# Optimization experiments

Hardware: AMD Instinct MI355X
Metric: run time of the kernel (lower is better)

The kernel has to match this reference:

```python
import jax, jax.numpy as jnp
import numpy as np

B, H, W, C = 4, 64, 64, 64
DK = C // 8  # key/query channels from Conv2D(filters=channels//8)


def setup_inputs() -> dict:
    key = jax.random.key(0)
    ks = jax.random.split(key, 4)
    x = jax.random.normal(ks[0], (B, H, W, C), dtype=jnp.float32)
    # he_normal-ish scale for 1x1 conv kernels (fan_in = C)
    s = np.sqrt(2.0 / C).astype(np.float32)
    Wf = jax.random.normal(ks[1], (C, DK), dtype=jnp.float32) * s
    Wg = jax.random.normal(ks[2], (C, DK), dtype=jnp.float32) * s
    Wh = jax.random.normal(ks[3], (C, C), dtype=jnp.float32) * s
    bf = jnp.zeros((DK,), dtype=jnp.float32)
    bg = jnp.zeros((DK,), dtype=jnp.float32)
    bh = jnp.zeros((C,), dtype=jnp.float32)
    return {"x": x, "Wf": Wf, "bf": bf, "Wg": Wg, "bg": bg, "Wh": Wh, "bh": bh}


def reference(x, Wf, bf, Wg, bg, Wh, bh):
    b, h, w, c = x.shape
    n = h * w
    xf = x.reshape(b, n, c)  # 1x1 conv == per-position linear over flattened spatial dims
    f = xf @ Wf + bf         # [B, N, DK]
    g = xf @ Wg + bg         # [B, N, DK]
    v = xf @ Wh + bh         # [B, N, C]
    # attention = softmax(g @ f^T) over keys (tf.nn.softmax default: last axis)
    scores = jnp.einsum('bnd,bmd->bnm', g, f)   # [B, N, N]
    attn = jax.nn.softmax(scores, axis=-1)
    out = jnp.einsum('bnm,bmc->bnc', attn, v)   # [B, N, C]
    return out
```

## Files before the change

kernel.cpp:

```cpp
#include <hip/hip_runtime.h>
#include <hip/hip_bf16.h>
#include <hip/hip_fp16.h>

typedef _Float16 half8_t  __attribute__((ext_vector_type(8)));
typedef short    short8_t __attribute__((ext_vector_type(8)));
typedef short    short4_t __attribute__((ext_vector_type(4)));
typedef float    f32x4    __attribute__((ext_vector_type(4)));

#define LOG2E 1.44269504088896f

__device__ __forceinline__ unsigned pack_bf16_2(float lo, float hi) {
  float2 f2; f2.x = lo; f2.y = hi;
  __hip_bfloat162 h2 = __float22bfloat162_rn(f2);
  return *reinterpret_cast<unsigned*>(&h2);
}

__global__ __launch_bounds__(256) void prep_kernel(
    const float* __restrict__ x,
    const float* __restrict__ Wf, const float* __restrict__ bf,
    const float* __restrict__ Wg, const float* __restrict__ bg,
    const float* __restrict__ Wh, const float* __restrict__ bh,
    _Float16* __restrict__ fh, _Float16* __restrict__ gh,
    unsigned short* __restrict__ vT)
{
  __shared__ _Float16 WtT[80 * 72];
  __shared__ float ball[80];
  const int t = threadIdx.x;

  for (int i = t; i < 512; i += 256) {
    int c = i >> 3, d = i & 7;
    WtT[d * 72 + c]       = (_Float16)Wf[i];
    WtT[(8 + d) * 72 + c] = (_Float16)(Wg[i] * LOG2E);
  }
  for (int i = t; i < 4096; i += 256) {
    int c = i >> 6, ch = i & 63;
    WtT[(16 + ch) * 72 + c] = (_Float16)Wh[i];
  }
  if (t < 80) ball[t] = (t < 8) ? bf[t] : (t < 16) ? bg[t - 8] * LOG2E : bh[t - 16];
  __syncthreads();

  const int lane = t & 63, w = t >> 6;
  const int quad = lane >> 4, l15 = lane & 15;
  const int p0 = blockIdx.x * 64;
  const int row = p0 + w * 16 + l15;

  const float* xr = x + (size_t)row * 64 + quad * 8;
  float4 xa = *(const float4*)(xr);
  float4 xb = *(const float4*)(xr + 4);
  float4 xc = *(const float4*)(xr + 32);
  float4 xd = *(const float4*)(xr + 36);
  half8_t a0, a1;
  a0[0]=(_Float16)xa.x; a0[1]=(_Float16)xa.y; a0[2]=(_Float16)xa.z; a0[3]=(_Float16)xa.w;
  a0[4]=(_Float16)xb.x; a0[5]=(_Float16)xb.y; a0[6]=(_Float16)xb.z; a0[7]=(_Float16)xb.w;
  a1[0]=(_Float16)xc.x; a1[1]=(_Float16)xc.y; a1[2]=(_Float16)xc.z; a1[3]=(_Float16)xc.w;
  a1[4]=(_Float16)xd.x; a1[5]=(_Float16)xd.y; a1[6]=(_Float16)xd.z; a1[7]=(_Float16)xd.w;

  const f32x4 zc = {0.f, 0.f, 0.f, 0.f};
  const int b     = p0 >> 12;
  const int nbase = (p0 & 4095) + w * 16 + quad * 4;
  const int kblock = nbase >> 5;
  const int r0     = nbase & 31;
  const int q8 = r0 >> 3, j8 = r0 & 7;
  const int slot0 = (j8 < 4) ? (q8 * 4 + j8) : (16 + q8 * 4 + (j8 - 4));
  const size_t fbase_out = ((size_t)b * 4096 + (kblock << 5) + slot0) * 8;
  const size_t gbase_out = ((size_t)p0 + w * 16 + quad * 4) * 8;
  const size_t vbase_out = (((size_t)b * 128 + kblock) << 11) + r0;

#pragma unroll
  for (int nt = 0; nt < 5; nt++) {
    const int ch0 = nt * 16 + l15;
    const _Float16* wt = &WtT[ch0 * 72 + quad * 8];
    half8_t b0 = *(const half8_t*)(wt);
    half8_t b1 = *(const half8_t*)(wt + 32);
    f32x4 d = __builtin_amdgcn_mfma_f32_16x16x32_f16(a0, b0, zc, 0, 0, 0);
    d = __builtin_amdgcn_mfma_f32_16x16x32_f16(a1, b1, d, 0, 0, 0);
    const float bias = ball[ch0];
    if (nt == 0) {
      if (l15 < 8) {
#pragma unroll
        for (int reg = 0; reg < 4; reg++)
          fh[fbase_out + (size_t)reg * 8 + l15] = (_Float16)(d[reg] + bias);
      } else {
#pragma unroll
        for (int reg = 0; reg < 4; reg++)
          gh[gbase_out + (size_t)reg * 8 + (l15 - 8)] = (_Float16)(d[reg] + bias);
      }
    } else {
      const int vch = ch0 - 16;
      union { unsigned u[2]; short4_t s; } pk;
      pk.u[0] = pack_bf16_2(d[0] + bias, d[1] + bias);
      pk.u[1] = pack_bf16_2(d[2] + bias, d[3] + bias);
      *(short4_t*)(vT + vbase_out + (size_t)vch * 32) = pk.s;
    }
  }
}

__device__ __forceinline__ void compute_chunk(
    const half8_t& f0, const half8_t& f1,
    const short8_t& v0, const short8_t& v1,
    const short8_t& v2, const short8_t& v3,
    const half8_t (&gfrag)[4], const short8_t& ones8,
    f32x4 (&acc)[4][4], f32x4 (&acc4)[4])
{
  const f32x4 zc = {0.f, 0.f, 0.f, 0.f};
#pragma unroll
  for (int tt = 0; tt < 4; tt++) {
    f32x4 s0 = __builtin_amdgcn_mfma_f32_16x16x32_f16(f0, gfrag[tt], zc, 0, 0, 0);
    f32x4 s1 = __builtin_amdgcn_mfma_f32_16x16x32_f16(f1, gfrag[tt], zc, 0, 0, 0);
    float p00 = __builtin_amdgcn_exp2f(s0[0]), p01 = __builtin_amdgcn_exp2f(s0[1]);
    float p02 = __builtin_amdgcn_exp2f(s0[2]), p03 = __builtin_amdgcn_exp2f(s0[3]);
    float p10 = __builtin_amdgcn_exp2f(s1[0]), p11 = __builtin_amdgcn_exp2f(s1[1]);
    float p12 = __builtin_amdgcn_exp2f(s1[2]), p13 = __builtin_amdgcn_exp2f(s1[3]);
    union { unsigned u[4]; short8_t v; } pu;
    pu.u[0] = pack_bf16_2(p00, p01);
    pu.u[1] = pack_bf16_2(p02, p03);
    pu.u[2] = pack_bf16_2(p10, p11);
    pu.u[3] = pack_bf16_2(p12, p13);
    short8_t pfrag = pu.v;
    acc[tt][0] = __builtin_amdgcn_mfma_f32_16x16x32_bf16(v0, pfrag, acc[tt][0], 0, 0, 0);
    acc[tt][1] = __builtin_amdgcn_mfma_f32_16x16x32_bf16(v1, pfrag, acc[tt][1], 0, 0, 0);
    acc[tt][2] = __builtin_amdgcn_mfma_f32_16x16x32_bf16(v2, pfrag, acc[tt][2], 0, 0, 0);
    acc[tt][3] = __builtin_amdgcn_mfma_f32_16x16x32_bf16(v3, pfrag, acc[tt][3], 0, 0, 0);
    acc4[tt]   = __builtin_amdgcn_mfma_f32_16x16x32_bf16(ones8, pfrag, acc4[tt], 0, 0, 0);
  }
}

__global__ __launch_bounds__(512, 2) void attn_kernel(
    const _Float16* __restrict__ fh,
    const _Float16* __restrict__ gh,
    const unsigned short* __restrict__ vT,
    float* __restrict__ out)
{
  const int N    = 4096;
  const int lane = threadIdx.x & 63;
  const int w    = threadIdx.x >> 6;
  const int quad = lane >> 4;
  const int l15  = lane & 15;

  __shared__ float red[7][64][17];

  const int xcd = blockIdx.x & 7;
  const int b   = xcd >> 1;
  const int qg  = ((blockIdx.x >> 3) << 1) + (xcd & 1);
  const int q0  = qg * 64;
  const int kbase = w * 512;
  const int phase = (qg >> 1) & 15;

  const _Float16* fbase = fh + (size_t)b * N * 8;
  const _Float16* gbase = gh + (size_t)b * N * 8;
  const short*    vbat  = (const short*)vT + (size_t)b * 262144 + (l15 << 5) + (quad << 3);

  half8_t gfrag[4] = {{}, {}, {}, {}};
  if (quad == 0) {
#pragma unroll
    for (int tt = 0; tt < 4; tt++)
      gfrag[tt] = *(const half8_t*)(gbase + (size_t)(q0 + tt * 16 + l15) * 8);
  }

  const f32x4 zc = {0.f, 0.f, 0.f, 0.f};
  f32x4 acc[4][4];
  f32x4 acc4[4];
#pragma unroll
  for (int tt = 0; tt < 4; tt++) {
    acc4[tt] = zc;
#pragma unroll
    for (int ct = 0; ct < 4; ct++) acc[tt][ct] = zc;
  }

  short8_t ones8;
#pragma unroll
  for (int i = 0; i < 8; i++) ones8[i] = (short)0x3F80;

  half8_t  fa0 = {}, fa1 = {}, fb0 = {}, fb1 = {};
  short8_t va0, va1, va2, va3, vb0, vb1, vb2, vb3;

  {
    const int k0 = kbase + (((0 + phase) & 15) << 5);
    if (quad == 0) {
      fa0 = *(const half8_t*)(fbase + (size_t)(k0 + l15) * 8);
      fa1 = *(const half8_t*)(fbase + (size_t)(k0 + 16 + l15) * 8);
    }
    const short* vk = vbat + ((size_t)(k0 >> 5) << 11);
    va0 = *(const short8_t*)(vk);
    va1 = *(const short8_t*)(vk + 512);
    va2 = *(const short8_t*)(vk + 1024);
    va3 = *(const short8_t*)(vk + 1536);
  }

#pragma unroll 1
  for (int cc = 0; cc < 16; cc += 2) {
    {
      const int k1 = kbase + (((cc + 1 + phase) & 15) << 5);
      if (quad == 0) {
        fb0 = *(const half8_t*)(fbase + (size_t)(k1 + l15) * 8);
        fb1 = *(const half8_t*)(fbase + (size_t)(k1 + 16 + l15) * 8);
      }
      const short* vk = vbat + ((size_t)(k1 >> 5) << 11);
      vb0 = *(const short8_t*)(vk);
      vb1 = *(const short8_t*)(vk + 512);
      vb2 = *(const short8_t*)(vk + 1024);
      vb3 = *(const short8_t*)(vk + 1536);
    }
    compute_chunk(fa0, fa1, va0, va1, va2, va3, gfrag, ones8, acc, acc4);
    if (cc + 2 < 16) {
      const int k2 = kbase + (((cc + 2 + phase) & 15) << 5);
      if (quad == 0) {
        fa0 = *(const half8_t*)(fbase + (size_t)(k2 + l15) * 8);
        fa1 = *(const half8_t*)(fbase + (size_t)(k2 + 16 + l15) * 8);
      }
      const short* vk = vbat + ((size_t)(k2 >> 5) << 11);
      va0 = *(const short8_t*)(vk);
      va1 = *(const short8_t*)(vk + 512);
      va2 = *(const short8_t*)(vk + 1024);
      va3 = *(const short8_t*)(vk + 1536);
    }
    compute_chunk(fb0, fb1, vb0, vb1, vb2, vb3, gfrag, ones8, acc, acc4);
  }

#pragma unroll 1
  for (int tt = 0; tt < 4; tt++) {
    if (w > 0) {
      float* p = &red[w - 1][lane][0];
#pragma unroll
      for (int ct = 0; ct < 4; ct++)
#pragma unroll
        for (int reg = 0; reg < 4; reg++) p[ct * 4 + reg] = acc[tt][ct][reg];
      p[16] = acc4[tt][0];
    }
    __syncthreads();
    if (w == 0) {
      f32x4 a0 = acc[tt][0], a1 = acc[tt][1], a2 = acc[tt][2], a3 = acc[tt][3];
      float lv = acc4[tt][0];
#pragma unroll
      for (int ww = 0; ww < 7; ww++) {
        const float* p = &red[ww][lane][0];
#pragma unroll
        for (int reg = 0; reg < 4; reg++) {
          a0[reg] += p[0 + reg];
          a1[reg] += p[4 + reg];
          a2[reg] += p[8 + reg];
          a3[reg] += p[12 + reg];
        }
        lv += p[16];
      }
      const float inv = 1.0f / lv;
      float* ob = out + ((size_t)b * N + q0 + tt * 16 + l15) * 64 + (quad << 2);
      *(f32x4*)(ob)      = a0 * inv;
      *(f32x4*)(ob + 16) = a1 * inv;
      *(f32x4*)(ob + 32) = a2 * inv;
      *(f32x4*)(ob + 48) = a3 * inv;
    }
    __syncthreads();
  }
}

extern "C" void kernel_launch(void* const* d_in, const int* in_sizes, int n_in,
                              void* d_out, int out_size, void* d_ws, size_t ws_size,
                              hipStream_t stream) {
  const float* x  = (const float*)d_in[0];
  const float* Wf = (const float*)d_in[1];
  const float* bf = (const float*)d_in[2];
  const float* Wg = (const float*)d_in[3];
  const float* bg = (const float*)d_in[4];
  const float* Wh = (const float*)d_in[5];
  const float* bh = (const float*)d_in[6];
  float* out = (float*)d_out;

  char* ws = (char*)d_ws;
  _Float16* fh = (_Float16*)ws;
  _Float16* gh = (_Float16*)(ws + 262144);
  unsigned short* vT = (unsigned short*)(ws + 524288);

  prep_kernel<<<256, 256, 0, stream>>>(x, Wf, bf, Wg, bg, Wh, bh, fh, gh, vT);
  attn_kernel<<<256, 512, 0, stream>>>(fh, gh, vT, out);
}
```

Before: 100.4 us.

## Fuse projection and attention kernels via cooperative launch with grid sync

Merges the 1x1-conv projection prep kernel into the attention kernel and launches a single cooperative kernel, with a grid-wide barrier between the projection phase and the attention phase. The projection work per block is split across 8 waves instead of 4, and the shared memory for the weight staging is reused as the reduction buffer. The aim is to remove the second launch and the gap between kernels. In exchange it adds a grid sync, and it requires all 256 blocks of 512 threads to be co-resident, which could fail or serialize if occupancy is lower.

```diff
diff --git a/kernel.cpp b/kernel.cpp
--- a/kernel.cpp
+++ b/kernel.cpp
@@ -1,4 +1,5 @@
 #include <hip/hip_runtime.h>
+#include <hip/hip_cooperative_groups.h>
 #include <hip/hip_bf16.h>
 #include <hip/hip_fp16.h>
 
@@ -13,86 +14,6 @@
   float2 f2; f2.x = lo; f2.y = hi;
   __hip_bfloat162 h2 = __float22bfloat162_rn(f2);
   return *reinterpret_cast<unsigned*>(&h2);
-}
-
-__global__ __launch_bounds__(256) void prep_kernel(
-    const float* __restrict__ x,
-    const float* __restrict__ Wf, const float* __restrict__ bf,
-    const float* __restrict__ Wg, const float* __restrict__ bg,
-    const float* __restrict__ Wh, const float* __restrict__ bh,
-    _Float16* __restrict__ fh, _Float16* __restrict__ gh,
-    unsigned short* __restrict__ vT)
-{
-  __shared__ _Float16 WtT[80 * 72];
-  __shared__ float ball[80];
-  const int t = threadIdx.x;
-
-  for (int i = t; i < 512; i += 256) {
-    int c = i >> 3, d = i & 7;
-    WtT[d * 72 + c]       = (_Float16)Wf[i];
-    WtT[(8 + d) * 72 + c] = (_Float16)(Wg[i] * LOG2E);
-  }
-  for (int i = t; i < 4096; i += 256) {
-    int c = i >> 6, ch = i & 63;
-    WtT[(16 + ch) * 72 + c] = (_Float16)Wh[i];
-  }
-  if (t < 80) ball[t] = (t < 8) ? bf[t] : (t < 16) ? bg[t - 8] * LOG2E : bh[t - 16];
-  __syncthreads();
-
-  const int lane = t & 63, w = t >> 6;
-  const int quad = lane >> 4, l15 = lane & 15;
-  const int p0 = blockIdx.x * 64;
-  const int row = p0 + w * 16 + l15;
-
-  const float* xr = x + (size_t)row * 64 + quad * 8;
-  float4 xa = *(const float4*)(xr);
-  float4 xb = *(const float4*)(xr + 4);
-  float4 xc = *(const float4*)(xr + 32);
-  float4 xd = *(const float4*)(xr + 36);
-  half8_t a0, a1;
-  a0[0]=(_Float16)xa.x; a0[1]=(_Float16)xa.y; a0[2]=(_Float16)xa.z; a0[3]=(_Float16)xa.w;
-  a0[4]=(_Float16)xb.x; a0[5]=(_Float16)xb.y; a0[6]=(_Float16)xb.z; a0[7]=(_Float16)xb.w;
-  a1[0]=(_Float16)xc.x; a1[1]=(_Float16)xc.y; a1[2]=(_Float16)xc.z; a1[3]=(_Float16)xc.w;
-  a1[4]=(_Float16)xd.x; a1[5]=(_Float16)xd.y; a1[6]=(_Float16)xd.z; a1[7]=(_Float16)xd.w;
-
-  const f32x4 zc = {0.f, 0.f, 0.f, 0.f};
-  const int b     = p0 >> 12;
-  const int nbase = (p0 & 4095) + w * 16 + quad * 4;
-  const int kblock = nbase >> 5;
-  const int r0     = nbase & 31;
-  const int q8 = r0 >> 3, j8 = r0 & 7;
-  const int slot0 = (j8 < 4) ? (q8 * 4 + j8) : (16 + q8 * 4 + (j8 - 4));
-  const size_t fbase_out = ((size_t)b * 4096 + (kblock << 5) + slot0) * 8;
-  const size_t gbase_out = ((size_t)p0 + w * 16 + quad * 4) * 8;
-  const size_t vbase_out = (((size_t)b * 128 + kblock) << 11) + r0;
-
-#pragma unroll
-  for (int nt = 0; nt < 5; nt++) {
-    const int ch0 = nt * 16 + l15;
-    const _Float16* wt = &WtT[ch0 * 72 + quad * 8];
-    half8_t b0 = *(const half8_t*)(wt);
-    half8_t b1 = *(const half8_t*)(wt + 32);
-    f32x4 d = __builtin_amdgcn_mfma_f32_16x16x32_f16(a0, b0, zc, 0, 0, 0);
-    d = __builtin_amdgcn_mfma_f32_16x16x32_f16(a1, b1, d, 0, 0, 0);
-    const float bias = ball[ch0];
-    if (nt == 0) {
-      if (l15 < 8) {
-#pragma unroll
-        for (int reg = 0; reg < 4; reg++)
-          fh[fbase_out + (size_t)reg * 8 + l15] = (_Float16)(d[reg] + bias);
-      } else {
-#pragma unroll
-        for (int reg = 0; reg < 4; reg++)
-          gh[gbase_out + (size_t)reg * 8 + (l15 - 8)] = (_Float16)(d[reg] + bias);
-      }
-    } else {
-      const int vch = ch0 - 16;
-      union { unsigned u[2]; short4_t s; } pk;
-      pk.u[0] = pack_bf16_2(d[0] + bias, d[1] + bias);
-      pk.u[1] = pack_bf16_2(d[2] + bias, d[3] + bias);
-      *(short4_t*)(vT + vbase_out + (size_t)vch * 32) = pk.s;
-    }
-  }
 }
 
 __device__ __forceinline__ void compute_chunk(
@@ -125,19 +46,126 @@
   }
 }
 
-__global__ __launch_bounds__(512, 2) void attn_kernel(
-    const _Float16* __restrict__ fh,
-    const _Float16* __restrict__ gh,
-    const unsigned short* __restrict__ vT,
+__global__ __launch_bounds__(512, 2) void fused_kernel(
+    const float* __restrict__ x,
+    const float* __restrict__ Wf, const float* __restrict__ bf,
+    const float* __restrict__ Wg, const float* __restrict__ bg,
+    const float* __restrict__ Wh, const float* __restrict__ bh,
+    _Float16* __restrict__ fh, _Float16* __restrict__ gh,
+    unsigned short* __restrict__ vT,
     float* __restrict__ out)
 {
-  const int N    = 4096;
-  const int lane = threadIdx.x & 63;
-  const int w    = threadIdx.x >> 6;
+  namespace cg = cooperative_groups;
+  __shared__ __align__(16) char smraw[7 * 64 * 17 * 4];
+
+  const int t    = threadIdx.x;
+  const int lane = t & 63;
+  const int wv   = t >> 6;
   const int quad = lane >> 4;
   const int l15  = lane & 15;
 
-  __shared__ float red[7][64][17];
+  {
+    _Float16* WtT = (_Float16*)smraw;
+    float*    ball = (float*)(smraw + 80 * 72 * 2);
+
+    {
+      int i = t;
+      int c = i >> 3, d = i & 7;
+      WtT[d * 72 + c]       = (_Float16)Wf[i];
+      WtT[(8 + d) * 72 + c] = (_Float16)(Wg[i] * LOG2E);
+    }
+    for (int i = t; i < 4096; i += 512) {
+      int c = i >> 6, ch = i & 63;
+      WtT[(16 + ch) * 72 + c] = (_Float16)Wh[i];
+    }
+    if (t < 80) ball[t] = (t < 8) ? bf[t] : (t < 16) ? bg[t - 8] * LOG2E : bh[t - 16];
+    __syncthreads();
+
+    const int wr   = wv & 3;
+    const int half = wv >> 2;
+    const int p0  = blockIdx.x * 64;
+    const int row = p0 + wr * 16 + l15;
+
+    const float* xr = x + (size_t)row * 64 + quad * 8;
+    float4 xa = *(const float4*)(xr);
+    float4 xb = *(const float4*)(xr + 4);
+    float4 xc = *(const float4*)(xr + 32);
+    float4 xd = *(const float4*)(xr + 36);
+    half8_t a0, a1;
+    a0[0]=(_Float16)xa.x; a0[1]=(_Float16)xa.y; a0[2]=(_Float16)xa.z; a0[3]=(_Float16)xa.w;
+    a0[4]=(_Float16)xb.x; a0[5]=(_Float16)xb.y; a0[6]=(_Float16)xb.z; a0[7]=(_Float16)xb.w;
+    a1[0]=(_Float16)xc.x; a1[1]=(_Float16)xc.y; a1[2]=(_Float16)xc.z; a1[3]=(_Float16)xc.w;
+    a1[4]=(_Float16)xd.x; a1[5]=(_Float16)xd.y; a1[6]=(_Float16)xd.z; a1[7]=(_Float16)xd.w;
+
+    const f32x4 zc = {0.f, 0.f, 0.f, 0.f};
+    const int b     = p0 >> 12;
+    const int nbase = (p0 & 4095) + wr * 16 + quad * 4;
+    const int kblock = nbase >> 5;
+    const int r0     = nbase & 31;
+    const int q8 = r0 >> 3, j8 = r0 & 7;
+    const int slot0 = (j8 < 4) ? (q8 * 4 + j8) : (16 + q8 * 4 + (j8 - 4));
+    const size_t fbase_out = ((size_t)b * 4096 + (kblock << 5) + slot0) * 8;
+    const size_t gbase_out = ((size_t)p0 + wr * 16 + quad * 4) * 8;
+    const size_t vbase_out = (((size_t)b * 128 + kblock) << 11) + r0;
+
+    if (half == 0) {
+      {
+        const _Float16* wt = &WtT[l15 * 72 + quad * 8];
+        half8_t b0 = *(const half8_t*)(wt);
+        half8_t b1 = *(const half8_t*)(wt + 32);
+        f32x4 d = __builtin_amdgcn_mfma_f32_16x16x32_f16(a0, b0, zc, 0, 0, 0);
+        d = __builtin_amdgcn_mfma_f32_16x16x32_f16(a1, b1, d, 0, 0, 0);
+        const float bias = ball[l15];
+        if (l15 < 8) {
+#pragma unroll
+          for (int reg = 0; reg < 4; reg++)
+            fh[fbase_out + (size_t)reg * 8 + l15] = (_Float16)(d[reg] + bias);
+        } else {
+#pragma unroll
+          for (int reg = 0; reg < 4; reg++)
+            gh[gbase_out + (size_t)reg * 8 + (l15 - 8)] = (_Float16)(d[reg] + bias);
+        }
+      }
+#pragma unroll
+      for (int nt = 1; nt < 3; nt++) {
+        const int ch0 = nt * 16 + l15;
+        const _Float16* wt = &WtT[ch0 * 72 + quad * 8];
+        half8_t b0 = *(const half8_t*)(wt);
+        half8_t b1 = *(const half8_t*)(wt + 32);
+        f32x4 d = __builtin_amdgcn_mfma_f32_16x16x32_f16(a0, b0, zc, 0, 0, 0);
+        d = __builtin_amdgcn_mfma_f32_16x16x32_f16(a1, b1, d, 0, 0, 0);
+        const float bias = ball[ch0];
+        const int vch = ch0 - 16;
+        union { unsigned u[2]; short4_t s; } pk;
+        pk.u[0] = pack_bf16_2(d[0] + bias, d[1] + bias);
+        pk.u[1] = pack_bf16_2(d[2] + bias, d[3] + bias);
+        *(short4_t*)(vT + vbase_out + (size_t)vch * 32) = pk.s;
+      }
+    } else {
+#pragma unroll
+      for (int nt = 3; nt < 5; nt++) {
+        const int ch0 = nt * 16 + l15;
+        const _Float16* wt = &WtT[ch0 * 72 + quad * 8];
+        half8_t b0 = *(const half8_t*)(wt);
+        half8_t b1 = *(const half8_t*)(wt + 32);
+        f32x4 d = __builtin_amdgcn_mfma_f32_16x16x32_f16(a0, b0, zc, 0, 0, 0);
+        d = __builtin_amdgcn_mfma_f32_16x16x32_f16(a1, b1, d, 0, 0, 0);
+        const float bias = ball[ch0];
+        const int vch = ch0 - 16;
+        union { unsigned u[2]; short4_t s; } pk;
+        pk.u[0] = pack_bf16_2(d[0] + bias, d[1] + bias);
+        pk.u[1] = pack_bf16_2(d[2] + bias, d[3] + bias);
+        *(short4_t*)(vT + vbase_out + (size_t)vch * 32) = pk.s;
+      }
+    }
+  }
+
+  __threadfence();
+  cg::this_grid().sync();
+
+  const int N    = 4096;
+  const int w    = wv;
+  float* red = (float*)smraw;
 
   const int xcd = blockIdx.x & 7;
   const int b   = xcd >> 1;
@@ -220,7 +248,7 @@
 #pragma unroll 1
   for (int tt = 0; tt < 4; tt++) {
     if (w > 0) {
-      float* p = &red[w - 1][lane][0];
+      float* p = &red[((w - 1) * 64 + lane) * 17];
 #pragma unroll
       for (int ct = 0; ct < 4; ct++)
 #pragma unroll
@@ -233,7 +261,7 @@
       float lv = acc4[tt][0];
 #pragma unroll
       for (int ww = 0; ww < 7; ww++) {
-        const float* p = &red[ww][lane][0];
+        const float* p = &red[(ww * 64 + lane) * 17];
 #pragma unroll
         for (int reg = 0; reg < 4; reg++) {
           a0[reg] += p[0 + reg];
@@ -271,6 +299,8 @@
   _Float16* gh = (_Float16*)(ws + 262144);
   unsigned short* vT = (unsigned short*)(ws + 524288);
 
-  prep_kernel<<<256, 256, 0, stream>>>(x, Wf, bf, Wg, bg, Wh, bh, fh, gh, vT);
-  attn_kernel<<<256, 512, 0, stream>>>(fh, gh, vT, out);
+  void* args[] = {(void*)&x, (void*)&Wf, (void*)&bf, (void*)&Wg, (void*)&bg,
+                  (void*)&Wh, (void*)&bh, (void*)&fh, (void*)&gh, (void*)&vT,
+                  (void*)&out};
+  hipLaunchCooperativeKernel((void*)fused_kernel, dim3(256), dim3(512), args, 0, stream);
 }
```

After: 193.9 us. 1.93x slower.
